# Optimization experiments

Hardware: AMD Instinct MI355X
Metric: run time of the kernel (lower is better)

Reference implementation:

```python
import jax, jax.numpy as jnp
import numpy as np

INPUT_SCALE = 1.0
RES_SCALE = 1.0
LEAK_RATE = 0.9


def setup_inputs() -> dict:
    key = jax.random.key(0)
    k1, k2, k3 = jax.random.split(key, 3)
    seq_len, input_size, res_size = 20000, 128, 2048
    input_data = jax.random.normal(k1, (seq_len, input_size), dtype=jnp.float32)
    W_in = jax.random.normal(k2, (res_size, input_size), dtype=jnp.float32)
    W_res = jax.random.normal(k3, (res_size, res_size), dtype=jnp.float32)
    return {"input_data": input_data, "W_in": W_in, "W_res": W_res}


def reference(input_data, W_in, W_res):
    res_size = W_res.shape[0]
    inv_sqrt_n = jnp.asarray(1.0 / np.sqrt(res_size), dtype=input_data.dtype)
    # Precompute the input projection for all timesteps: [T, R]
    proj = INPUT_SCALE * jnp.einsum('ti,ri->tr', input_data, W_in)

    def step(x_prev, p_t):
        pre = p_t + RES_SCALE * (W_res @ x_prev)
        x = (1.0 - LEAK_RATE) * x_prev + LEAK_RATE * jax.lax.erf(pre) * inv_sqrt_n
        return x, x

    x0 = jnp.zeros((res_size,), dtype=input_data.dtype)
    _, xs = jax.lax.scan(step, x0, proj)
    return xs  # [seq_len, res_size]
```

## Files before the change

### kernel.cpp

```cpp
#include <hip/hip_runtime.h>
#include <math.h>

#define T_STEPS 20000
#define RSIZE   2048
#define ISIZE   128
#define NBLK    64
#define NTHR    512
#define RPW     4
#define FSTRIDE 16

__device__ __forceinline__ float erf_approx(float x) {
    float ax = fabsf(x);
    float t  = 1.0f / (1.0f + 0.3275911f * ax);
    float y  = t * (0.254829592f +
               t * (-0.284496736f +
               t * (1.421413741f +
               t * (-1.453152027f +
               t * 1.061405429f))));
    float e  = __expf(-ax * ax);
    float r  = 1.0f - y * e;
    return copysignf(r, x);
}

#define AGPR_W(a, v) asm volatile("v_accvgpr_write_b32 %0, %1" : "=a"(a) : "v"(v))
#define AGPR_R(v, a) asm volatile("v_accvgpr_read_b32 %0, %1" : "=v"(v) : "a"(a))

__device__ __forceinline__ unsigned ld_coh_u32(const unsigned* p) {
    unsigned r;
    asm volatile("global_load_dword %0, %1, off sc0 sc1\n\ts_waitcnt vmcnt(0)"
                 : "=v"(r) : "v"(p) : "memory");
    return r;
}
__device__ __forceinline__ float4 ld_coh_f4(const float* p) {
    float4 r;
    asm volatile("global_load_dwordx4 %0, %1, off sc0 sc1\n\ts_waitcnt vmcnt(0)"
                 : "=v"(r) : "v"(p) : "memory");
    return r;
}
__device__ __forceinline__ void st_coh_f32(float* p, float v) {
    asm volatile("global_store_dword %0, %1, off sc0 sc1"
                 :: "v"(p), "v"(v) : "memory");
}
__device__ __forceinline__ void st_coh_u32(unsigned* p, unsigned v) {
    asm volatile("global_store_dword %0, %1, off sc0 sc1"
                 :: "v"(p), "v"(v) : "memory");
}

__global__ __launch_bounds__(NTHR, 2) void esn_persistent(
        const float* __restrict__ input,
        const float* __restrict__ W_in,
        const float* __restrict__ W_res,
        float* __restrict__ out,
        unsigned* __restrict__ flags) {
    __shared__ float xbuf[RSIZE];

    const int tid  = threadIdx.x;
    const int lane = tid & 63;
    const int wv   = tid >> 6;
    const int wid  = blockIdx.x * (NTHR / 64) + wv;
    const int r0   = wid * RPW;
    const float invs = 0.022097086912079608f;

    float a_w[RPW][32];
    float a_wi[RPW][2];
#pragma unroll
    for (int m = 0; m < RPW; ++m) {
        const float* row = W_res + (size_t)(r0 + m) * RSIZE;
#pragma unroll
        for (int c = 0; c < 8; ++c) {
            float4 w = *(const float4*)(row + c * 256 + lane * 4);
            AGPR_W(a_w[m][c * 4 + 0], w.x);
            AGPR_W(a_w[m][c * 4 + 1], w.y);
            AGPR_W(a_w[m][c * 4 + 2], w.z);
            AGPR_W(a_w[m][c * 4 + 3], w.w);
        }
        float2 wiv = *(const float2*)(W_in + (size_t)(r0 + m) * ISIZE + lane * 2);
        AGPR_W(a_wi[m][0], wiv.x);
        AGPR_W(a_wi[m][1], wiv.y);
    }

    unsigned*       myflag   = flags + blockIdx.x * FSTRIDE;
    const unsigned* pollflag = flags + lane * FSTRIDE;

    for (int t = 0; t < T_STEPS; ++t) {
        float2 uv = ((const float2*)(input + (size_t)t * ISIZE))[lane];
        float base[RPW];
#pragma unroll
        for (int m = 0; m < RPW; ++m) {
            float w0, w1;
            AGPR_R(w0, a_wi[m][0]);
            AGPR_R(w1, a_wi[m][1]);
            base[m] = w0 * uv.x + w1 * uv.y;
        }

        float4 xv[8];
        float  xp = 0.0f;
        if (t > 0) {
            if (wv == 0) {
                const unsigned want = (unsigned)t;
                while (true) {
                    unsigned f = ld_coh_u32(pollflag);
                    if (__all((int)(f >= want))) break;
                    __builtin_amdgcn_s_sleep(1);
                }
            }
            __syncthreads();
            const float* xprev = out + (size_t)(t - 1) * RSIZE;
            ((float4*)xbuf)[tid] = ld_coh_f4(xprev + tid * 4);
            __syncthreads();
#pragma unroll
            for (int c = 0; c < 8; ++c)
                xv[c] = ((const float4*)xbuf)[c * 64 + lane];
            if (lane < RPW) xp = xbuf[r0 + lane];
        } else {
#pragma unroll
            for (int c = 0; c < 8; ++c)
                xv[c] = make_float4(0.f, 0.f, 0.f, 0.f);
        }

        float acc[RPW];
#pragma unroll
        for (int m = 0; m < RPW; ++m) {
            float s0 = base[m];
            float s1 = 0.0f;
#pragma unroll
            for (int c = 0; c < 8; ++c) {
                float t0, t1, t2, t3;
                AGPR_R(t0, a_w[m][c * 4 + 0]);
                AGPR_R(t1, a_w[m][c * 4 + 1]);
                AGPR_R(t2, a_w[m][c * 4 + 2]);
                AGPR_R(t3, a_w[m][c * 4 + 3]);
                s0 = fmaf(t0, xv[c].x, s0);
                s1 = fmaf(t1, xv[c].y, s1);
                s0 = fmaf(t2, xv[c].z, s0);
                s1 = fmaf(t3, xv[c].w, s1);
            }
            float a = s0 + s1;
#pragma unroll
            for (int off = 32; off > 0; off >>= 1)
                a += __shfl_xor(a, off, 64);
            acc[m] = a;
        }

        if (lane < RPW) {
            float pre = (lane == 0) ? acc[0]
                      : (lane == 1) ? acc[1]
                      : (lane == 2) ? acc[2] : acc[3];
            float xn  = 0.1f * xp + 0.9f * erf_approx(pre) * invs;
            st_coh_f32(out + (size_t)t * RSIZE + r0 + lane, xn);
        }
        asm volatile("s_waitcnt vmcnt(0)" ::: "memory");
        __syncthreads();
        if (tid == 0)
            st_coh_u32(myflag, (unsigned)(t + 1));
    }
}

extern "C" void kernel_launch(void* const* d_in, const int* in_sizes, int n_in,
                              void* d_out, int out_size, void* d_ws,
                              size_t ws_size, hipStream_t stream) {
    const float* input = (const float*)d_in[0];
    const float* W_in  = (const float*)d_in[1];
    const float* W_res = (const float*)d_in[2];
    float*       out   = (float*)d_out;
    unsigned*    flags = (unsigned*)d_ws;

    hipMemsetAsync(flags, 0, NBLK * FSTRIDE * sizeof(unsigned), stream);

    void* args[] = {(void*)&input, (void*)&W_in, (void*)&W_res,
                    (void*)&out, (void*)&flags};
    hipError_t err = hipLaunchCooperativeKernel(
        (const void*)esn_persistent, dim3(NBLK), dim3(NTHR), args, 0, stream);
    if (err != hipSuccess) {
        esn_persistent<<<dim3(NBLK), dim3(NTHR), 0, stream>>>(
            input, W_in, W_res, out, flags);
    }
}
```

Baseline: 61.87 ms.

## Replace per-step block barrier with per-wave polling and LDS arrival counter

Each wave now polls its own replicated copy of the per-block step flags, so the block barrier before the poll goes away. The barrier at the end of a step is replaced by an LDS atomic arrival counter: the last wave to arrive publishes the step flag to all per-wave copies. The matvec loop is also reordered so the four row accumulators interleave across chunks, which gives more independent FMA chains. This removes two block-wide syncs per step but adds more polling traffic (eight waves per block poll) and more flag stores.

```diff
diff --git a/kernel.cpp b/kernel.cpp
--- a/kernel.cpp
+++ b/kernel.cpp
@@ -6,8 +6,8 @@
 #define ISIZE   128
 #define NBLK    64
 #define NTHR    512
+#define WPB     (NTHR / 64)
 #define RPW     4
-#define FSTRIDE 16
 
 __device__ __forceinline__ float erf_approx(float x) {
     float ax = fabsf(x);
@@ -28,13 +28,13 @@
 __device__ __forceinline__ unsigned ld_coh_u32(const unsigned* p) {
     unsigned r;
     asm volatile("global_load_dword %0, %1, off sc0 sc1\n\ts_waitcnt vmcnt(0)"
-                 : "=v"(r) : "v"(p) : "memory");
+                 : "=&v"(r) : "v"(p) : "memory");
     return r;
 }
 __device__ __forceinline__ float4 ld_coh_f4(const float* p) {
     float4 r;
     asm volatile("global_load_dwordx4 %0, %1, off sc0 sc1\n\ts_waitcnt vmcnt(0)"
-                 : "=v"(r) : "v"(p) : "memory");
+                 : "=&v"(r) : "v"(p) : "memory");
     return r;
 }
 __device__ __forceinline__ void st_coh_f32(float* p, float v) {
@@ -53,11 +53,12 @@
         float* __restrict__ out,
         unsigned* __restrict__ flags) {
     __shared__ float xbuf[RSIZE];
+    __shared__ unsigned cnt;
 
     const int tid  = threadIdx.x;
     const int lane = tid & 63;
     const int wv   = tid >> 6;
-    const int wid  = blockIdx.x * (NTHR / 64) + wv;
+    const int wid  = blockIdx.x * WPB + wv;
     const int r0   = wid * RPW;
     const float invs = 0.022097086912079608f;
 
@@ -78,64 +79,60 @@
         AGPR_W(a_wi[m][0], wiv.x);
         AGPR_W(a_wi[m][1], wiv.y);
     }
-
-    unsigned*       myflag   = flags + blockIdx.x * FSTRIDE;
-    const unsigned* pollflag = flags + lane * FSTRIDE;
+    if (tid == 0) cnt = 0;
+    __syncthreads();
 
     for (int t = 0; t < T_STEPS; ++t) {
         float2 uv = ((const float2*)(input + (size_t)t * ISIZE))[lane];
-        float base[RPW];
+        float acc[RPW];
 #pragma unroll
         for (int m = 0; m < RPW; ++m) {
             float w0, w1;
             AGPR_R(w0, a_wi[m][0]);
             AGPR_R(w1, a_wi[m][1]);
-            base[m] = w0 * uv.x + w1 * uv.y;
+            acc[m] = fmaf(w0, uv.x, w1 * uv.y);
         }
 
-        float4 xv[8];
-        float  xp = 0.0f;
         if (t > 0) {
-            if (wv == 0) {
-                const unsigned want = (unsigned)t;
-                while (true) {
-                    unsigned f = ld_coh_u32(pollflag);
-                    if (__all((int)(f >= want))) break;
-                    __builtin_amdgcn_s_sleep(1);
-                }
+            const unsigned want = (unsigned)t;
+            const unsigned* pf = flags + wv * NBLK + lane;
+            while (true) {
+                unsigned f = ld_coh_u32(pf);
+                if (__all((int)(f >= want))) break;
+                __builtin_amdgcn_s_sleep(1);
             }
-            __syncthreads();
             const float* xprev = out + (size_t)(t - 1) * RSIZE;
             ((float4*)xbuf)[tid] = ld_coh_f4(xprev + tid * 4);
-            __syncthreads();
+        } else {
+            ((float4*)xbuf)[tid] = make_float4(0.f, 0.f, 0.f, 0.f);
+        }
+        __syncthreads();
+
+        float4 xv[8];
 #pragma unroll
-            for (int c = 0; c < 8; ++c)
-                xv[c] = ((const float4*)xbuf)[c * 64 + lane];
-            if (lane < RPW) xp = xbuf[r0 + lane];
-        } else {
+        for (int c = 0; c < 8; ++c)
+            xv[c] = ((const float4*)xbuf)[c * 64 + lane];
+        float xp = xbuf[r0 + (lane & 3)];
+
 #pragma unroll
-            for (int c = 0; c < 8; ++c)
-                xv[c] = make_float4(0.f, 0.f, 0.f, 0.f);
-        }
-
-        float acc[RPW];
+        for (int c = 0; c < 8; ++c) {
 #pragma unroll
-        for (int m = 0; m < RPW; ++m) {
-            float s0 = base[m];
-            float s1 = 0.0f;
-#pragma unroll
-            for (int c = 0; c < 8; ++c) {
+            for (int m = 0; m < RPW; ++m) {
                 float t0, t1, t2, t3;
                 AGPR_R(t0, a_w[m][c * 4 + 0]);
                 AGPR_R(t1, a_w[m][c * 4 + 1]);
                 AGPR_R(t2, a_w[m][c * 4 + 2]);
                 AGPR_R(t3, a_w[m][c * 4 + 3]);
-                s0 = fmaf(t0, xv[c].x, s0);
-                s1 = fmaf(t1, xv[c].y, s1);
-                s0 = fmaf(t2, xv[c].z, s0);
-                s1 = fmaf(t3, xv[c].w, s1);
+                float p0 = fmaf(t0, xv[c].x, acc[m]);
+                float p1 = t1 * xv[c].y;
+                float p2 = fmaf(t2, xv[c].z, p0);
+                float p3 = fmaf(t3, xv[c].w, p1);
+                acc[m] = p2 + p3;
             }
-            float a = s0 + s1;
+        }
+#pragma unroll
+        for (int m = 0; m < RPW; ++m) {
+            float a = acc[m];
 #pragma unroll
             for (int off = 32; off > 0; off >>= 1)
                 a += __shfl_xor(a, off, 64);
@@ -149,10 +146,20 @@
             float xn  = 0.1f * xp + 0.9f * erf_approx(pre) * invs;
             st_coh_f32(out + (size_t)t * RSIZE + r0 + lane, xn);
         }
-        asm volatile("s_waitcnt vmcnt(0)" ::: "memory");
-        __syncthreads();
-        if (tid == 0)
-            st_coh_u32(myflag, (unsigned)(t + 1));
+
+        if (t + 1 < T_STEPS) {
+            asm volatile("s_waitcnt vmcnt(0)" ::: "memory");
+            if (lane == 0) {
+                unsigned ret = __hip_atomic_fetch_add(&cnt, 1u, __ATOMIC_ACQ_REL,
+                                                      __HIP_MEMORY_SCOPE_WORKGROUP);
+                if (ret == 8u * (unsigned)t + 7u) {
+#pragma unroll
+                    for (int w = 0; w < WPB; ++w)
+                        st_coh_u32(flags + w * NBLK + blockIdx.x,
+                                   (unsigned)(t + 1));
+                }
+            }
+        }
     }
 }
 
@@ -165,7 +172,7 @@
     float*       out   = (float*)d_out;
     unsigned*    flags = (unsigned*)d_ws;
 
-    hipMemsetAsync(flags, 0, NBLK * FSTRIDE * sizeof(unsigned), stream);
+    hipMemsetAsync(flags, 0, WPB * NBLK * sizeof(unsigned), stream);
 
     void* args[] = {(void*)&input, (void*)&W_in, (void*)&W_res,
                     (void*)&out, (void*)&flags};
```

After: 130.1 ms. 2.1x slower.
